# Performance work log

Hardware: AMD Instinct MI355X
Metric: run time of the kernel (lower is better)

Reference implementation:

```python
import jax, jax.numpy as jnp
import numpy as np

B, N, F, P, HID, OUT = 4, 20000, 8, 12, 64, 1
E = 320000


def _glorot(k, shape):
    lim = float(np.sqrt(6.0 / (shape[0] + shape[1])))
    return jax.random.uniform(k, shape, jnp.float32, -lim, lim)


def setup_inputs() -> dict:
    key = jax.random.key(0)
    ks = jax.random.split(key, 20)
    inp = {
        "x": jax.random.normal(ks[0], (B, N, F, P), jnp.float32),
        "edge_index": jax.random.randint(ks[1], (2, E), 0, N, jnp.int64),
        "edge_attr": jax.random.uniform(ks[2], (E,), jnp.float32),
        # GCNConv weights (stored [in, out]) + biases for z, r, h gates
        "conv_z_w": _glorot(ks[3], (F, HID)), "conv_z_b": jnp.zeros((HID,), jnp.float32),
        "conv_r_w": _glorot(ks[4], (F, HID)), "conv_r_b": jnp.zeros((HID,), jnp.float32),
        "conv_h_w": _glorot(ks[5], (F, HID)), "conv_h_b": jnp.zeros((HID,), jnp.float32),
        # GRU linear layers on cat([conv_out, H]) -> HID (stored [in, out])
        "lin_z_w": _glorot(ks[6], (2 * HID, HID)), "lin_z_b": jnp.zeros((HID,), jnp.float32),
        "lin_r_w": _glorot(ks[7], (2 * HID, HID)), "lin_r_b": jnp.zeros((HID,), jnp.float32),
        "lin_h_w": _glorot(ks[8], (2 * HID, HID)), "lin_h_b": jnp.zeros((HID,), jnp.float32),
        # temporal attention logits over periods
        "attention": jax.random.uniform(ks[9], (P,), jnp.float32),
        # final linear: HID -> OUT*P
        "out_w": _glorot(ks[10], (HID, OUT * P)), "out_b": jnp.zeros((OUT * P,), jnp.float32),
    }
    return inp


def reference(x, edge_index, edge_attr,
              conv_z_w, conv_z_b, conv_r_w, conv_r_b, conv_h_w, conv_h_b,
              lin_z_w, lin_z_b, lin_r_w, lin_r_b, lin_h_w, lin_h_b,
              attention, out_w, out_b):
    Bb, Nn, Ff, Pp = x.shape
    Hh = conv_z_w.shape[1]

    # GCN normalization with self loops: A_hat = D^-1/2 (A + I) D^-1/2
    loop = jnp.arange(Nn)
    row = jnp.concatenate([edge_index[0], loop])
    col = jnp.concatenate([edge_index[1], loop])
    w = jnp.concatenate([edge_attr, jnp.ones((Nn,), x.dtype)])
    deg = jax.ops.segment_sum(w, col, num_segments=Nn)
    dinv = jnp.where(deg > 0, jax.lax.rsqrt(deg), 0.0)
    norm = dinv[row] * w * dinv[col]  # [E+N]

    def gcn(xt, W, b):
        # xt: [B, N, F] -> [B, N, H]
        xw = jnp.einsum('bnf,fh->bnh', xt, W)
        msg = xw[:, row, :] * norm[None, :, None]            # gather over source nodes
        agg = jax.vmap(lambda m: jax.ops.segment_sum(m, col, num_segments=Nn))(msg)
        return agg + b

    H0 = jnp.zeros((Bb, Nn, Hh), x.dtype)  # A3TGCN2 passes H=None each period -> zeros

    def tgcn_cell(xt):
        Z = jax.nn.sigmoid(jnp.concatenate([gcn(xt, conv_z_w, conv_z_b), H0], -1) @ lin_z_w + lin_z_b)
        R = jax.nn.sigmoid(jnp.concatenate([gcn(xt, conv_r_w, conv_r_b), H0], -1) @ lin_r_w + lin_r_b)
        Ht = jnp.tanh(jnp.concatenate([gcn(xt, conv_h_w, conv_h_b), H0 * R], -1) @ lin_h_w + lin_h_b)
        return Z * H0 + (1.0 - Z) * Ht

    probs = jax.nn.softmax(attention)
    xs = jnp.moveaxis(x, -1, 0)  # [P, B, N, F]

    def step(acc, inp):
        xt, p = inp
        return acc + p * tgcn_cell(xt), None

    h_accum, _ = jax.lax.scan(step, jnp.zeros((Bb, Nn, Hh), x.dtype), (xs, probs))

    h = jax.nn.relu(h_accum)
    out = h @ out_w + out_b                 # [B, N, OUT*P]
    return out.reshape(Bb, Nn, -1, Pp)      # [B, N, OUT, P]
```

## Files before the change

### kernel.cpp

```cpp
#include <hip/hip_runtime.h>

#define NN 20000
#define EE 320000
#define CAP 64
#define SVC 72
#define OVCAP 8192
#define EBLK 1250

#define WZ_O 0
#define BZ_O 512
#define WH_O 576
#define BH_O 1088
#define OWT_O 1152
#define OB_O 1968
#define PR_O 1980

#define LOG2E 1.44269504088896340736f

typedef float v2f __attribute__((ext_vector_type(2)));

__device__ __forceinline__ v2f mk2(float a, float b) { v2f t; t.x = a; t.y = b; return t; }
__device__ __forceinline__ v2f pkfma(v2f a, v2f b, v2f c) {
  v2f d;
  asm("v_pk_fma_f32 %0, %1, %2, %3" : "=v"(d) : "v"(a), "v"(b), "v"(c));
  return d;
}
__device__ __forceinline__ v2f pkmul(v2f a, v2f b) {
  v2f d;
  asm("v_pk_mul_f32 %0, %1, %2" : "=v"(d) : "v"(a), "v"(b));
  return d;
}

__device__ __forceinline__ float b2f(unsigned short h) {
  union { unsigned int u; float f; } v; v.u = ((unsigned int)h) << 16; return v.f;
}
__device__ __forceinline__ unsigned short f2b(float f) {
  union { unsigned int u; float f; } v; v.f = f;
  unsigned int u = v.u;
  unsigned int r = (u + 0x7fffu + ((u >> 16) & 1u)) >> 16;
  return (unsigned short)r;
}
__device__ __forceinline__ float ldw(const void* p, int i, int isbf) {
  return isbf ? b2f(((const unsigned short*)p)[i]) : ((const float*)p)[i];
}
__device__ __forceinline__ float degf(unsigned long long dc) {
  return (float)(unsigned int)dc * (1.0f / 1048576.0f);
}
__device__ __forceinline__ float ex2(float x) {
#if __has_builtin(__builtin_amdgcn_exp2f)
  return __builtin_amdgcn_exp2f(x);
#else
  return __exp2f(x);
#endif
}
__device__ __forceinline__ v2f bpk(unsigned int u) {
  union { unsigned int i; float f; } lo, hi;
  lo.i = u << 16; hi.i = u & 0xffff0000u;
  return mk2(lo.f, hi.f);
}

struct __align__(4) U3 { unsigned int x, y, z; };

__global__ void __launch_bounds__(256) k_append(
    const void* __restrict__ ei, const void* __restrict__ ea,
    unsigned long long* __restrict__ degcnt,
    unsigned int* __restrict__ slab,
    int* __restrict__ ovf_cnt, int* __restrict__ ovf_dst,
    unsigned int* __restrict__ ovf_pack, float* __restrict__ consts,
    const void* czw, const void* czb, const void* chw, const void* chb,
    const void* lzw, const void* lzb, const void* lhw, const void* lhb,
    const void* att, const void* ow, const void* ob) {
  __shared__ int sfl[2];
  const int tid = threadIdx.x;
  if (tid < 64) {
    unsigned long long b1 = __ballot((((const unsigned int*)ea)[tid] >> 15) & 1u);
    unsigned long long b2 = __ballot(((const unsigned int*)ei)[2 * tid + 1] != 0u);
    if (tid == 0) {
      sfl[0] = (b1 == 0ull) ? 1 : 0;
      sfl[1] = (b2 == 0ull) ? 1 : 0;
    }
  }
  __syncthreads();
  const int isbf = sfl[0], is64 = sfl[1];

  if (blockIdx.x == EBLK) {
    for (int idx = tid; idx < 512; idx += 256) {
      int f = idx >> 6, k = idx & 63;
      float sz = 0.f, sh = 0.f;
      for (int h = 0; h < 64; ++h) {
        sz += ldw(czw, f * 64 + h, isbf) * ldw(lzw, h * 64 + k, isbf);
        sh += ldw(chw, f * 64 + h, isbf) * ldw(lhw, h * 64 + k, isbf);
      }
      consts[WZ_O + idx] = sz * LOG2E;
      consts[WH_O + idx] = sh * (2.0f * LOG2E);
    }
    for (int idx = tid; idx < 64; idx += 256) {
      float sz = ldw(lzb, idx, isbf), sh = ldw(lhb, idx, isbf);
      for (int h = 0; h < 64; ++h) {
        sz += ldw(czb, h, isbf) * ldw(lzw, h * 64 + idx, isbf);
        sh += ldw(chb, h, isbf) * ldw(lhw, h * 64 + idx, isbf);
      }
      consts[BZ_O + idx] = sz * LOG2E;
      consts[BH_O + idx] = sh * (2.0f * LOG2E);
    }
    for (int idx = tid; idx < 816; idx += 256) {
      int p = idx / 68, kk = idx % 68;
      consts[OWT_O + idx] = (kk < 64) ? ldw(ow, kk * 12 + p, isbf) : 0.f;
    }
    if (tid < 12) consts[OB_O + tid] = ldw(ob, tid, isbf);
    if (tid == 0) {
      float a[12]; float m = -1e30f;
      for (int p = 0; p < 12; ++p) { a[p] = ldw(att, p, isbf); m = fmaxf(m, a[p]); }
      float ssum = 0.f;
      for (int p = 0; p < 12; ++p) { a[p] = __expf(a[p] - m); ssum += a[p]; }
      for (int p = 0; p < 12; ++p) consts[PR_O + p] = a[p] / ssum;
    }
    return;
  }

  const int e = blockIdx.x * 256 + tid;
  if (e < EE) {
    int r, c;
    if (is64) {
      r = (int)((const unsigned int*)ei)[2 * e];
      c = (int)((const unsigned int*)ei)[2 * (EE + e)];
    } else {
      r = ((const int*)ei)[e];
      c = ((const int*)ei)[EE + e];
    }
    unsigned short wb;
    float wv;
    if (isbf) { wb = ((const unsigned short*)ea)[e]; wv = b2f(wb); }
    else      { wv = ((const float*)ea)[e]; wb = f2b(wv); }
    unsigned long long pk = (1ull << 32) |
        (unsigned long long)(unsigned int)__float2int_rn(wv * 1048576.0f);
    unsigned long long old = atomicAdd(&degcnt[c], pk);
    int pos = (int)(old >> 32);
    unsigned int packed = ((unsigned int)wb << 16) | (unsigned int)r;
    if (pos < CAP) {
      slab[c * CAP + pos] = packed;
    } else {
      int oi = atomicAdd(ovf_cnt, 1);
      if (oi < OVCAP) { ovf_dst[oi] = c; ovf_pack[oi] = packed; }
    }
  }
}

#define ACC6P(u, vv)                              \
  { aa0 = pkfma(bpk((u).x), vv, aa0);             \
    aa1 = pkfma(bpk((u).y), vv, aa1);             \
    aa2 = pkfma(bpk((u).z), vv, aa2); }

__global__ void __launch_bounds__(256) k_node(
    const void* __restrict__ x, const void* __restrict__ ea,
    const unsigned long long* __restrict__ degcnt,
    const unsigned int* __restrict__ slab,
    const int* __restrict__ ovf_cnt, const int* __restrict__ ovf_dst,
    const unsigned int* __restrict__ ovf_pack,
    const float* __restrict__ consts,
    void* __restrict__ out) {
  __shared__ __align__(16) float sow[840];
  __shared__ __align__(16) int2  sv[4 * SVC];
  __shared__ __align__(16) float accT[4 * 384];
  __shared__ __align__(16) float hw[4 * 272];
  __shared__ int swcnt[4];
  __shared__ int sfl[1];

  const int tid  = threadIdx.x;
  const int w    = tid >> 6;
  const int lane = tid & 63;
  const int n    = blockIdx.x * 4 + w;

  if (tid < 64) {
    unsigned long long b1 = __ballot((((const unsigned int*)ea)[tid] >> 15) & 1u);
    if (tid == 0) sfl[0] = (b1 == 0ull) ? 1 : 0;
  }
  for (int i = tid; i < 840; i += 256) sow[i] = consts[OWT_O + i];
  v2f wzp[4], whp[4];
#pragma unroll
  for (int j = 0; j < 4; ++j) {
    wzp[j] = mk2(consts[WZ_O + (2 * j) * 64 + lane], consts[WZ_O + (2 * j + 1) * 64 + lane]);
    whp[j] = mk2(consts[WH_O + (2 * j) * 64 + lane], consts[WH_O + (2 * j + 1) * 64 + lane]);
  }
  const float bz = consts[BZ_O + lane], bh = consts[BH_O + lane];
  __syncthreads();
  const int isbf = sfl[0];

  unsigned long long dcn = degcnt[n];
  int cnt = (int)(dcn >> 32);
  int base = cnt < CAP ? cnt : CAP;
  const float dn = rsqrtf(degf(dcn) + 1.0f);
  int2* svw = &sv[w * SVC];
  if (lane == 0) swcnt[w] = base;
  if (lane < base) {
    unsigned int pk = slab[n * CAP + lane];
    int s = (int)(pk & 0xffffu);
    float v = b2f((unsigned short)(pk >> 16)) * rsqrtf(degf(degcnt[s]) + 1.0f) * dn;
    svw[lane] = make_int2(s * 96, __float_as_int(v));
  }
  int m0 = base;
  {
    int ov = ovf_cnt[0];
    if (ov > 0) {
      if (ov > OVCAP) ov = OVCAP;
      for (int i = lane; i < ov; i += 64) {
        if (ovf_dst[i] == n) {
          int idx = atomicAdd(&swcnt[w], 1);
          if (idx < SVC - 1) {
            unsigned int pk = ovf_pack[i];
            int s = (int)(pk & 0xffffu);
            float v = b2f((unsigned short)(pk >> 16)) *
                      rsqrtf(degf(degcnt[s]) + 1.0f) * dn;
            svw[idx] = make_int2(s * 96, __float_as_int(v));
          }
        }
      }
      __builtin_amdgcn_wave_barrier();
      m0 = swcnt[w];
      if (m0 > SVC - 1) m0 = SVC - 1;
    }
  }
  if (lane == 0) svw[m0] = make_int2(n * 96, __float_as_int(dn * dn));
  const int m1 = m0 + 1;
  __builtin_amdgcn_wave_barrier();

  v2f aa0 = mk2(0.f, 0.f), aa1 = mk2(0.f, 0.f), aa2 = mk2(0.f, 0.f);
  {
    const int i15 = lane & 15;
    const long xbase = (long)(lane >> 4) * (NN * 96) + 6 * i15;
    if (isbf) {
      const unsigned short* xr = (const unsigned short*)x + xbase;
      int j = 0;
      for (; j + 1 < m1; j += 2) {
        int2 e0 = svw[j], e1 = svw[j + 1];
        U3 u0 = *(const U3*)(xr + e0.x);
        U3 u1 = *(const U3*)(xr + e1.x);
        v2f vv0 = mk2(__int_as_float(e0.y), __int_as_float(e0.y));
        v2f vv1 = mk2(__int_as_float(e1.y), __int_as_float(e1.y));
        ACC6P(u0, vv0); ACC6P(u1, vv1);
      }
      if (j < m1) {
        int2 e0 = svw[j];
        U3 u0 = *(const U3*)(xr + e0.x);
        v2f vv0 = mk2(__int_as_float(e0.y), __int_as_float(e0.y));
        ACC6P(u0, vv0);
      }
    } else {
      const float* xf = (const float*)x + xbase;
      int j = 0;
      for (; j + 1 < m1; j += 2) {
        int2 e0 = svw[j], e1 = svw[j + 1];
        const v2f* p0 = (const v2f*)(xf + e0.x);
        const v2f* p1 = (const v2f*)(xf + e1.x);
        v2f u00 = p0[0], u01 = p0[1], u02 = p0[2];
        v2f u10 = p1[0], u11 = p1[1], u12 = p1[2];
        v2f vv0 = mk2(__int_as_float(e0.y), __int_as_float(e0.y));
        v2f vv1 = mk2(__int_as_float(e1.y), __int_as_float(e1.y));
        aa0 = pkfma(u00, vv0, aa0); aa1 = pkfma(u01, vv0, aa1); aa2 = pkfma(u02, vv0, aa2);
        aa0 = pkfma(u10, vv1, aa0); aa1 = pkfma(u11, vv1, aa1); aa2 = pkfma(u12, vv1, aa2);
      }
      if (j < m1) {
        int2 e0 = svw[j];
        const v2f* p0 = (const v2f*)(xf + e0.x);
        v2f vv0 = mk2(__int_as_float(e0.y), __int_as_float(e0.y));
        aa0 = pkfma(p0[0], vv0, aa0); aa1 = pkfma(p0[1], vv0, aa1); aa2 = pkfma(p0[2], vv0, aa2);
      }
    }
    float* aw = &accT[w * 384 + (lane >> 4) * 96 + (i15 & 1) * 48 + (i15 >> 1)];
    aw[0]  = aa0.x; aw[8]  = aa0.y;
    aw[16] = aa1.x; aw[24] = aa1.y;
    aw[32] = aa2.x; aw[40] = aa2.y;
  }
  __builtin_amdgcn_wave_barrier();

  {
    const float* accTw = &accT[w * 384];
    float* hww = &hw[w * 272];
    float prv[12];
#pragma unroll
    for (int p = 0; p < 12; ++p) prv[p] = sow[828 + p];
#pragma unroll
    for (int b = 0; b < 4; ++b) {
      float hbl = 0.f;
#pragma unroll
      for (int p = 0; p < 12; ++p) {
        const float4* A = (const float4*)&accTw[b * 96 + p * 8];
        float4 A0 = A[0], A1 = A[1];
        v2f zv = pkmul(mk2(A0.x, A0.y), wzp[0]);
        zv = pkfma(mk2(A0.z, A0.w), wzp[1], zv);
        zv = pkfma(mk2(A1.x, A1.y), wzp[2], zv);
        zv = pkfma(mk2(A1.z, A1.w), wzp[3], zv);
        v2f tv = pkmul(mk2(A0.x, A0.y), whp[0]);
        tv = pkfma(mk2(A0.z, A0.w), whp[1], tv);
        tv = pkfma(mk2(A1.x, A1.y), whp[2], tv);
        tv = pkfma(mk2(A1.z, A1.w), whp[3], tv);
        float za = zv.x + zv.y + bz;
        float ta = tv.x + tv.y + bh;
        float ea2 = ex2(za);
        float eh = ex2(fminf(ta, 115.0f));
        float num = eh - 1.0f;
        float den = (1.0f + ea2) * (1.0f + eh);
        hbl += prv[p] * (num * __builtin_amdgcn_rcpf(den));
      }
      hww[b * 68 + lane] = fmaxf(hbl, 0.f);
    }
  }
  __builtin_amdgcn_wave_barrier();

  if (lane < 48) {
    const float* hww = &hw[w * 272];
    int b = lane / 12, p = lane % 12;
    v2f acc2 = mk2(0.f, 0.f);
#pragma unroll
    for (int kq = 0; kq < 16; ++kq) {
      float4 hv = *(const float4*)&hww[b * 68 + 4 * kq];
      float4 wv = *(const float4*)&sow[p * 68 + 4 * kq];
      acc2 = pkfma(mk2(hv.x, hv.y), mk2(wv.x, wv.y), acc2);
      acc2 = pkfma(mk2(hv.z, hv.w), mk2(wv.z, wv.w), acc2);
    }
    float o = acc2.x + acc2.y + sow[816 + p];
    int oi = (b * NN + n) * 12 + p;
    if (isbf) ((unsigned short*)out)[oi] = f2b(o);
    else      ((float*)out)[oi] = o;
  }
}

extern "C" void kernel_launch(void* const* d_in, const int* in_sizes, int n_in,
                              void* d_out, int out_size, void* d_ws, size_t ws_size,
                              hipStream_t stream) {
  const void* x   = d_in[0];
  const void* ei  = d_in[1];
  const void* ea  = d_in[2];
  const void* czw = d_in[3];
  const void* czb = d_in[4];
  const void* chw = d_in[7];
  const void* chb = d_in[8];
  const void* lzw = d_in[9];
  const void* lzb = d_in[10];
  const void* lhw = d_in[13];
  const void* lhb = d_in[14];
  const void* att = d_in[15];
  const void* ow  = d_in[16];
  const void* ob  = d_in[17];

  char* ws = (char*)d_ws;
  float* consts  = (float*)(ws + 256);
  unsigned long long* degcnt = (unsigned long long*)(ws + 8448);
  int*   ovf_cnt = (int*)  (ws + 168448);
  int*   ovf_dst = (int*)  (ws + 168704);
  unsigned int* ovf_pack = (unsigned int*)(ws + 201472);
  unsigned int* slab     = (unsigned int*)(ws + 234240);

  hipMemsetAsync(ws + 8448, 0, 160064, stream);
  k_append<<<dim3(EBLK + 1), dim3(256), 0, stream>>>(ei, ea, degcnt, slab,
                                                     ovf_cnt, ovf_dst, ovf_pack,
                                                     consts,
                                                     czw, czb, chw, chb,
                                                     lzw, lzb, lhw, lhb,
                                                     att, ow, ob);
  k_node<<<dim3(NN / 4), dim3(256), 0, stream>>>(x, ea, degcnt, slab,
                                                 ovf_cnt, ovf_dst, ovf_pack,
                                                 consts, d_out);
}
```

Baseline: 229.5 us.

## Software-pipeline bf16 neighbor gather and hoist slab/degree loads before barrier

The bf16 gather loop becomes a double-buffered, 8-deep software pipeline: the next batch of 8 neighbor rows is loaded while the current batch is accumulated, to hide global-load latency. The slab entry and source-degree loads are issued before the block barrier so they overlap the constant loading. The fp32 path switches to scalar FMAs and the attention epilogue reads accT as v2f pairs. In exchange, register pressure rises from 16 buffered U3 values, which may hurt occupancy, and the unconditional slab read adds an out-of-range clamp.

```diff
diff --git a/kernel.cpp b/kernel.cpp
--- a/kernel.cpp
+++ b/kernel.cpp
@@ -146,10 +146,27 @@
   }
 }
 
-#define ACC6P(u, vv)                              \
-  { aa0 = pkfma(bpk((u).x), vv, aa0);             \
-    aa1 = pkfma(bpk((u).y), vv, aa1);             \
-    aa2 = pkfma(bpk((u).z), vv, aa2); }
+#define ACCF6(f0, f1, f2, v)                                                   \
+  { af[0] += (v) * (f0).x; af[1] += (v) * (f0).y; af[2] += (v) * (f1).x;       \
+    af[3] += (v) * (f1).y; af[4] += (v) * (f2).x; af[5] += (v) * (f2).y; }
+
+#define LD1(S, k, base)                                                        \
+  if ((base) + (k) < m1) {                                                     \
+    int2 t_ = svw[(base) + (k)];                                               \
+    v##S##k = __int_as_float(t_.y);                                            \
+    u##S##k = *(const U3*)(xr + t_.x);                                         \
+  }
+#define CO1(S, k, base)                                                        \
+  if ((base) + (k) < m1) {                                                     \
+    v2f vv_ = mk2(v##S##k, v##S##k);                                           \
+    aa0 = pkfma(bpk(u##S##k.x), vv_, aa0);                                     \
+    aa1 = pkfma(bpk(u##S##k.y), vv_, aa1);                                     \
+    aa2 = pkfma(bpk(u##S##k.z), vv_, aa2);                                     \
+  }
+#define LD8M(S, base) LD1(S,0,base) LD1(S,1,base) LD1(S,2,base) LD1(S,3,base) \
+                      LD1(S,4,base) LD1(S,5,base) LD1(S,6,base) LD1(S,7,base)
+#define CO8M(S, base) CO1(S,0,base) CO1(S,1,base) CO1(S,2,base) CO1(S,3,base) \
+                      CO1(S,4,base) CO1(S,5,base) CO1(S,6,base) CO1(S,7,base)
 
 __global__ void __launch_bounds__(256) k_node(
     const void* __restrict__ x, const void* __restrict__ ea,
@@ -171,6 +188,9 @@
   const int lane = tid & 63;
   const int n    = blockIdx.x * 4 + w;
 
+  unsigned long long dcn = degcnt[n];
+  unsigned int pk0 = slab[n * CAP + lane];
+
   if (tid < 64) {
     unsigned long long b1 = __ballot((((const unsigned int*)ea)[tid] >> 15) & 1u);
     if (tid == 0) sfl[0] = (b1 == 0ull) ? 1 : 0;
@@ -183,20 +203,22 @@
     whp[j] = mk2(consts[WH_O + (2 * j) * 64 + lane], consts[WH_O + (2 * j + 1) * 64 + lane]);
   }
   const float bz = consts[BZ_O + lane], bh = consts[BH_O + lane];
+
+  int s0 = (int)(pk0 & 0xffffu);
+  if (s0 >= NN) s0 = 0;
+  unsigned long long dgs = degcnt[s0];
+
   __syncthreads();
   const int isbf = sfl[0];
 
-  unsigned long long dcn = degcnt[n];
   int cnt = (int)(dcn >> 32);
   int base = cnt < CAP ? cnt : CAP;
   const float dn = rsqrtf(degf(dcn) + 1.0f);
   int2* svw = &sv[w * SVC];
   if (lane == 0) swcnt[w] = base;
   if (lane < base) {
-    unsigned int pk = slab[n * CAP + lane];
-    int s = (int)(pk & 0xffffu);
-    float v = b2f((unsigned short)(pk >> 16)) * rsqrtf(degf(degcnt[s]) + 1.0f) * dn;
-    svw[lane] = make_int2(s * 96, __float_as_int(v));
+    float v = b2f((unsigned short)(pk0 >> 16)) * rsqrtf(degf(dgs) + 1.0f) * dn;
+    svw[lane] = make_int2(s0 * 96, __float_as_int(v));
   }
   int m0 = base;
   {
@@ -230,41 +252,45 @@
     const long xbase = (long)(lane >> 4) * (NN * 96) + 6 * i15;
     if (isbf) {
       const unsigned short* xr = (const unsigned short*)x + xbase;
+      U3 uA0, uA1, uA2, uA3, uA4, uA5, uA6, uA7;
+      U3 uB0, uB1, uB2, uB3, uB4, uB5, uB6, uB7;
+      float vA0, vA1, vA2, vA3, vA4, vA5, vA6, vA7;
+      float vB0, vB1, vB2, vB3, vB4, vB5, vB6, vB7;
       int j = 0;
-      for (; j + 1 < m1; j += 2) {
-        int2 e0 = svw[j], e1 = svw[j + 1];
-        U3 u0 = *(const U3*)(xr + e0.x);
-        U3 u1 = *(const U3*)(xr + e1.x);
-        v2f vv0 = mk2(__int_as_float(e0.y), __int_as_float(e0.y));
-        v2f vv1 = mk2(__int_as_float(e1.y), __int_as_float(e1.y));
-        ACC6P(u0, vv0); ACC6P(u1, vv1);
-      }
-      if (j < m1) {
-        int2 e0 = svw[j];
-        U3 u0 = *(const U3*)(xr + e0.x);
-        v2f vv0 = mk2(__int_as_float(e0.y), __int_as_float(e0.y));
-        ACC6P(u0, vv0);
+      LD8M(A, 0)
+      for (;;) {
+        LD8M(B, j + 8)
+        CO8M(A, j)
+        j += 8;
+        if (j >= m1) break;
+        LD8M(A, j + 8)
+        CO8M(B, j)
+        j += 8;
+        if (j >= m1) break;
       }
     } else {
+      float af[6];
+#pragma unroll
+      for (int t = 0; t < 6; ++t) af[t] = 0.f;
       const float* xf = (const float*)x + xbase;
       int j = 0;
       for (; j + 1 < m1; j += 2) {
         int2 e0 = svw[j], e1 = svw[j + 1];
-        const v2f* p0 = (const v2f*)(xf + e0.x);
-        const v2f* p1 = (const v2f*)(xf + e1.x);
-        v2f u00 = p0[0], u01 = p0[1], u02 = p0[2];
-        v2f u10 = p1[0], u11 = p1[1], u12 = p1[2];
-        v2f vv0 = mk2(__int_as_float(e0.y), __int_as_float(e0.y));
-        v2f vv1 = mk2(__int_as_float(e1.y), __int_as_float(e1.y));
-        aa0 = pkfma(u00, vv0, aa0); aa1 = pkfma(u01, vv0, aa1); aa2 = pkfma(u02, vv0, aa2);
-        aa0 = pkfma(u10, vv1, aa0); aa1 = pkfma(u11, vv1, aa1); aa2 = pkfma(u12, vv1, aa2);
+        const float2* p0 = (const float2*)(xf + e0.x);
+        const float2* p1 = (const float2*)(xf + e1.x);
+        float2 u00 = p0[0], u01 = p0[1], u02 = p0[2];
+        float2 u10 = p1[0], u11 = p1[1], u12 = p1[2];
+        float v0 = __int_as_float(e0.y), v1 = __int_as_float(e1.y);
+        ACCF6(u00, u01, u02, v0); ACCF6(u10, u11, u12, v1);
       }
       if (j < m1) {
         int2 e0 = svw[j];
-        const v2f* p0 = (const v2f*)(xf + e0.x);
-        v2f vv0 = mk2(__int_as_float(e0.y), __int_as_float(e0.y));
-        aa0 = pkfma(p0[0], vv0, aa0); aa1 = pkfma(p0[1], vv0, aa1); aa2 = pkfma(p0[2], vv0, aa2);
-      }
+        const float2* p0 = (const float2*)(xf + e0.x);
+        float2 u00 = p0[0], u01 = p0[1], u02 = p0[2];
+        float v0 = __int_as_float(e0.y);
+        ACCF6(u00, u01, u02, v0);
+      }
+      aa0 = mk2(af[0], af[1]); aa1 = mk2(af[2], af[3]); aa2 = mk2(af[4], af[5]);
     }
     float* aw = &accT[w * 384 + (lane >> 4) * 96 + (i15 & 1) * 48 + (i15 >> 1)];
     aw[0]  = aa0.x; aw[8]  = aa0.y;
@@ -284,16 +310,16 @@
       float hbl = 0.f;
 #pragma unroll
       for (int p = 0; p < 12; ++p) {
-        const float4* A = (const float4*)&accTw[b * 96 + p * 8];
-        float4 A0 = A[0], A1 = A[1];
-        v2f zv = pkmul(mk2(A0.x, A0.y), wzp[0]);
-        zv = pkfma(mk2(A0.z, A0.w), wzp[1], zv);
-        zv = pkfma(mk2(A1.x, A1.y), wzp[2], zv);
-        zv = pkfma(mk2(A1.z, A1.w), wzp[3], zv);
-        v2f tv = pkmul(mk2(A0.x, A0.y), whp[0]);
-        tv = pkfma(mk2(A0.z, A0.w), whp[1], tv);
-        tv = pkfma(mk2(A1.x, A1.y), whp[2], tv);
-        tv = pkfma(mk2(A1.z, A1.w), whp[3], tv);
+        const v2f* A2 = (const v2f*)&accTw[b * 96 + p * 8];
+        v2f a01 = A2[0], a23 = A2[1], a45 = A2[2], a67 = A2[3];
+        v2f zv = pkmul(a01, wzp[0]);
+        zv = pkfma(a23, wzp[1], zv);
+        zv = pkfma(a45, wzp[2], zv);
+        zv = pkfma(a67, wzp[3], zv);
+        v2f tv = pkmul(a01, whp[0]);
+        tv = pkfma(a23, whp[1], tv);
+        tv = pkfma(a45, whp[2], tv);
+        tv = pkfma(a67, whp[3], tv);
         float za = zv.x + zv.y + bz;
         float ta = tv.x + tv.y + bh;
         float ea2 = ex2(za);
```

Result: slower. 236.9 us (+3.2%).

## Transpose bf16 x into node-major workspace copy for contiguous gathers

Applied to the files above, without the earlier changes.

Adds extra blocks to the append kernel that copy bf16 x from [B][N][96] into a node-major [N][B*96] workspace buffer, so each gathered neighbor row becomes one contiguous 768-byte segment instead of four strided pieces. The node kernel then indexes this buffer when the workspace is large enough and the input is bf16. The fp32 path swaps packed FMAs for scalar FMAs, and the LDS reads in the gate loop change from float4 to v2f. In exchange it adds a full read and write of x per call and depends on the workspace size check.

```diff
diff --git a/kernel.cpp b/kernel.cpp
--- a/kernel.cpp
+++ b/kernel.cpp
@@ -6,6 +6,7 @@
 #define SVC 72
 #define OVCAP 8192
 #define EBLK 1250
+#define NTB 256
 
 #define WZ_O 0
 #define BZ_O 512
@@ -62,6 +63,7 @@
 struct __align__(4) U3 { unsigned int x, y, z; };
 
 __global__ void __launch_bounds__(256) k_append(
+    const void* __restrict__ x, unsigned short* __restrict__ xt, int wsok,
     const void* __restrict__ ei, const void* __restrict__ ea,
     unsigned long long* __restrict__ degcnt,
     unsigned int* __restrict__ slab,
@@ -118,6 +120,21 @@
     return;
   }
 
+  if (blockIdx.x > EBLK) {
+    if (!(wsok && isbf)) return;
+    const uint4* xs = (const uint4*)x;
+    uint4* xd = (uint4*)xt;
+    const int t0 = (blockIdx.x - (EBLK + 1)) * 256 + tid;
+    for (int i = t0; i < 960000; i += NTB * 256) {
+      int n = i / 48;
+      int t = i - n * 48;
+      int b = t / 12;
+      int c8 = t - b * 12;
+      xd[i] = xs[b * 240000 + n * 12 + c8];
+    }
+    return;
+  }
+
   const int e = blockIdx.x * 256 + tid;
   if (e < EE) {
     int r, c;
@@ -151,8 +168,13 @@
     aa1 = pkfma(bpk((u).y), vv, aa1);             \
     aa2 = pkfma(bpk((u).z), vv, aa2); }
 
+#define ACCF6(f0, f1, f2, v)                                                   \
+  { af[0] += (v) * (f0).x; af[1] += (v) * (f0).y; af[2] += (v) * (f1).x;       \
+    af[3] += (v) * (f1).y; af[4] += (v) * (f2).x; af[5] += (v) * (f2).y; }
+
 __global__ void __launch_bounds__(256) k_node(
-    const void* __restrict__ x, const void* __restrict__ ea,
+    const void* __restrict__ x, const unsigned short* __restrict__ xt, int wsok,
+    const void* __restrict__ ea,
     const unsigned long long* __restrict__ degcnt,
     const unsigned int* __restrict__ slab,
     const int* __restrict__ ovf_cnt, const int* __restrict__ ovf_dst,
@@ -185,6 +207,8 @@
   const float bz = consts[BZ_O + lane], bh = consts[BH_O + lane];
   __syncthreads();
   const int isbf = sfl[0];
+  const int use_xt = wsok & isbf;
+  const int scale = use_xt ? 384 : 96;
 
   unsigned long long dcn = degcnt[n];
   int cnt = (int)(dcn >> 32);
@@ -196,7 +220,7 @@
     unsigned int pk = slab[n * CAP + lane];
     int s = (int)(pk & 0xffffu);
     float v = b2f((unsigned short)(pk >> 16)) * rsqrtf(degf(degcnt[s]) + 1.0f) * dn;
-    svw[lane] = make_int2(s * 96, __float_as_int(v));
+    svw[lane] = make_int2(s * scale, __float_as_int(v));
   }
   int m0 = base;
   {
@@ -211,7 +235,7 @@
             int s = (int)(pk & 0xffffu);
             float v = b2f((unsigned short)(pk >> 16)) *
                       rsqrtf(degf(degcnt[s]) + 1.0f) * dn;
-            svw[idx] = make_int2(s * 96, __float_as_int(v));
+            svw[idx] = make_int2(s * scale, __float_as_int(v));
           }
         }
       }
@@ -220,16 +244,17 @@
       if (m0 > SVC - 1) m0 = SVC - 1;
     }
   }
-  if (lane == 0) svw[m0] = make_int2(n * 96, __float_as_int(dn * dn));
+  if (lane == 0) svw[m0] = make_int2(n * scale, __float_as_int(dn * dn));
   const int m1 = m0 + 1;
   __builtin_amdgcn_wave_barrier();
 
   v2f aa0 = mk2(0.f, 0.f), aa1 = mk2(0.f, 0.f), aa2 = mk2(0.f, 0.f);
   {
     const int i15 = lane & 15;
-    const long xbase = (long)(lane >> 4) * (NN * 96) + 6 * i15;
     if (isbf) {
-      const unsigned short* xr = (const unsigned short*)x + xbase;
+      const unsigned short* xr =
+          use_xt ? (xt + lane * 6)
+                 : ((const unsigned short*)x + (long)(lane >> 4) * (NN * 96) + 6 * i15);
       int j = 0;
       for (; j + 1 < m1; j += 2) {
         int2 e0 = svw[j], e1 = svw[j + 1];
@@ -246,25 +271,28 @@
         ACC6P(u0, vv0);
       }
     } else {
-      const float* xf = (const float*)x + xbase;
+      float af[6];
+#pragma unroll
+      for (int t = 0; t < 6; ++t) af[t] = 0.f;
+      const float* xf = (const float*)x + (long)(lane >> 4) * (NN * 96) + 6 * i15;
       int j = 0;
       for (; j + 1 < m1; j += 2) {
         int2 e0 = svw[j], e1 = svw[j + 1];
-        const v2f* p0 = (const v2f*)(xf + e0.x);
-        const v2f* p1 = (const v2f*)(xf + e1.x);
-        v2f u00 = p0[0], u01 = p0[1], u02 = p0[2];
-        v2f u10 = p1[0], u11 = p1[1], u12 = p1[2];
-        v2f vv0 = mk2(__int_as_float(e0.y), __int_as_float(e0.y));
-        v2f vv1 = mk2(__int_as_float(e1.y), __int_as_float(e1.y));
-        aa0 = pkfma(u00, vv0, aa0); aa1 = pkfma(u01, vv0, aa1); aa2 = pkfma(u02, vv0, aa2);
-        aa0 = pkfma(u10, vv1, aa0); aa1 = pkfma(u11, vv1, aa1); aa2 = pkfma(u12, vv1, aa2);
+        const float2* p0 = (const float2*)(xf + e0.x);
+        const float2* p1 = (const float2*)(xf + e1.x);
+        float2 u00 = p0[0], u01 = p0[1], u02 = p0[2];
+        float2 u10 = p1[0], u11 = p1[1], u12 = p1[2];
+        float v0 = __int_as_float(e0.y), v1 = __int_as_float(e1.y);
+        ACCF6(u00, u01, u02, v0); ACCF6(u10, u11, u12, v1);
       }
       if (j < m1) {
         int2 e0 = svw[j];
-        const v2f* p0 = (const v2f*)(xf + e0.x);
-        v2f vv0 = mk2(__int_as_float(e0.y), __int_as_float(e0.y));
-        aa0 = pkfma(p0[0], vv0, aa0); aa1 = pkfma(p0[1], vv0, aa1); aa2 = pkfma(p0[2], vv0, aa2);
-      }
+        const float2* p0 = (const float2*)(xf + e0.x);
+        float2 u00 = p0[0], u01 = p0[1], u02 = p0[2];
+        float v0 = __int_as_float(e0.y);
+        ACCF6(u00, u01, u02, v0);
+      }
+      aa0 = mk2(af[0], af[1]); aa1 = mk2(af[2], af[3]); aa2 = mk2(af[4], af[5]);
     }
     float* aw = &accT[w * 384 + (lane >> 4) * 96 + (i15 & 1) * 48 + (i15 >> 1)];
     aw[0]  = aa0.x; aw[8]  = aa0.y;
@@ -284,16 +312,16 @@
       float hbl = 0.f;
 #pragma unroll
       for (int p = 0; p < 12; ++p) {
-        const float4* A = (const float4*)&accTw[b * 96 + p * 8];
-        float4 A0 = A[0], A1 = A[1];
-        v2f zv = pkmul(mk2(A0.x, A0.y), wzp[0]);
-        zv = pkfma(mk2(A0.z, A0.w), wzp[1], zv);
-        zv = pkfma(mk2(A1.x, A1.y), wzp[2], zv);
-        zv = pkfma(mk2(A1.z, A1.w), wzp[3], zv);
-        v2f tv = pkmul(mk2(A0.x, A0.y), whp[0]);
-        tv = pkfma(mk2(A0.z, A0.w), whp[1], tv);
-        tv = pkfma(mk2(A1.x, A1.y), whp[2], tv);
-        tv = pkfma(mk2(A1.z, A1.w), whp[3], tv);
+        const v2f* A2 = (const v2f*)&accTw[b * 96 + p * 8];
+        v2f a01 = A2[0], a23 = A2[1], a45 = A2[2], a67 = A2[3];
+        v2f zv = pkmul(a01, wzp[0]);
+        zv = pkfma(a23, wzp[1], zv);
+        zv = pkfma(a45, wzp[2], zv);
+        zv = pkfma(a67, wzp[3], zv);
+        v2f tv = pkmul(a01, whp[0]);
+        tv = pkfma(a23, whp[1], tv);
+        tv = pkfma(a45, whp[2], tv);
+        tv = pkfma(a67, whp[3], tv);
         float za = zv.x + zv.y + bz;
         float ta = tv.x + tv.y + bh;
         float ea2 = ex2(za);
@@ -350,15 +378,15 @@
   int*   ovf_dst = (int*)  (ws + 168704);
   unsigned int* ovf_pack = (unsigned int*)(ws + 201472);
   unsigned int* slab     = (unsigned int*)(ws + 234240);
+  unsigned short* xtp    = (unsigned short*)(ws + 5356544);
+
+  const int wsok = (ws_size >= 20716544u) ? 1 : 0;
 
   hipMemsetAsync(ws + 8448, 0, 160064, stream);
-  k_append<<<dim3(EBLK + 1), dim3(256), 0, stream>>>(ei, ea, degcnt, slab,
-                                                     ovf_cnt, ovf_dst, ovf_pack,
-                                                     consts,
-                                                     czw, czb, chw, chb,
-                                                     lzw, lzb, lhw, lhb,
-                                                     att, ow, ob);
-  k_node<<<dim3(NN / 4), dim3(256), 0, stream>>>(x, ea, degcnt, slab,
+  k_append<<<dim3(EBLK + 1 + NTB), dim3(256), 0, stream>>>(
+      x, xtp, wsok, ei, ea, degcnt, slab, ovf_cnt, ovf_dst, ovf_pack, consts,
+      czw, czb, chw, chb, lzw, lzb, lhw, lhb, att, ow, ob);
+  k_node<<<dim3(NN / 4), dim3(256), 0, stream>>>(x, xtp, wsok, ea, degcnt, slab,
                                                  ovf_cnt, ovf_dst, ovf_pack,
                                                  consts, d_out);
 }
```

Result: slower. 234.8 us (+2.3%).
